# Optimization experiments

Hardware: AMD Instinct MI355X
Metric: run time of the kernel (lower is better)

Reference implementation:

```python
import jax, jax.numpy as jnp
import numpy as np

N = 500_000
EPS = 1e-5  # torch BatchNorm1d default eps

def _lin(x, w, b):
    # Conv1d(k=1) / Linear over per-point features: x [N,Cin], w [Cout,Cin]
    return x @ w.T + b

def _bn(x, g, b):
    # training-mode BatchNorm1d with batch=1: stats over the N points per channel
    m = jnp.mean(x, axis=0)
    v = jnp.mean((x - m) ** 2, axis=0)  # biased variance, as torch uses for normalization
    return g * (x - m) * jax.lax.rsqrt(v + EPS) + b

def _fuse(f3d, f2d, w2d, b2d, w3d, b3d, watt, batt):
    # AttentionalFuser: tanh/sigmoid gated fusion, output channels = 2*C
    d2d = _lin(f2d, w2d, b2d)                      # [N,C]
    mid = jnp.tanh(_lin(f3d, w3d, b3d) + d2d)      # [N,C]
    att = jax.nn.sigmoid(_lin(mid, watt, batt))    # [N,C]
    return jnp.concatenate([f3d, att * d2d], axis=1)  # [N,2C]

def setup_inputs() -> dict:
    key = jax.random.key(0)
    ks = iter(jax.random.split(key, 64))
    def rn(*shape):
        return jax.random.normal(next(ks), shape, dtype=jnp.float32) * 0.1
    inp = {"points": jax.random.normal(next(ks), (N, 10), dtype=jnp.float32)}
    for i, c in zip(range(1, 5), [8, 16, 32, 64]):
        inp[f"f2d_{i}"] = jax.random.normal(next(ks), (N, c), dtype=jnp.float32)
    for i, (o, ci) in enumerate([(8, 6), (16, 16), (32, 32), (64, 64), (256, 128)], 1):
        inp[f"w_c{i}"] = rn(o, ci); inp[f"b_c{i}"] = rn(o)
    for i, c in zip(range(1, 6), [16, 32, 64, 128, 256]):
        inp[f"g{i}"] = jnp.ones((c,), jnp.float32); inp[f"be{i}"] = jnp.zeros((c,), jnp.float32)
    for i, c in zip(range(1, 5), [8, 16, 32, 64]):
        inp[f"w2d_{i}"] = rn(c, c); inp[f"b2d_{i}"] = rn(c)
        inp[f"w3d_{i}"] = rn(c, c); inp[f"b3d_{i}"] = rn(c)
        inp[f"watt_{i}"] = rn(c, c); inp[f"batt_{i}"] = rn(c)
    return inp

def reference(points, f2d_1, f2d_2, f2d_3, f2d_4,
              w_c1, b_c1, w_c2, b_c2, w_c3, b_c3, w_c4, b_c4, w_c5, b_c5,
              g1, be1, g2, be2, g3, be3, g4, be4, g5, be5,
              w2d_1, b2d_1, w3d_1, b3d_1, watt_1, batt_1,
              w2d_2, b2d_2, w3d_2, b3d_2, watt_2, batt_2,
              w2d_3, b2d_3, w3d_3, b3d_3, watt_3, batt_3,
              w2d_4, b2d_4, w3d_4, b3d_4, watt_4, batt_4):
    x = jnp.concatenate([points[:, 0:3], points[:, 7:10]], axis=1)  # [N,6] pos+RGB
    x = jax.nn.relu(_lin(x, w_c1, b_c1))                            # [N,8]
    x = _bn(_fuse(x, f2d_1, w2d_1, b2d_1, w3d_1, b3d_1, watt_1, batt_1), g1, be1)  # [N,16]
    x = jax.nn.relu(_lin(x, w_c2, b_c2))                            # [N,16]
    x = _bn(_fuse(x, f2d_2, w2d_2, b2d_2, w3d_2, b3d_2, watt_2, batt_2), g2, be2)  # [N,32]
    x = jax.nn.relu(_lin(x, w_c3, b_c3))                            # [N,32]
    x = _bn(_fuse(x, f2d_3, w2d_3, b2d_3, w3d_3, b3d_3, watt_3, batt_3), g3, be3)  # [N,64]
    point_feature = x                                               # [N,64]
    x = jax.nn.relu(_lin(x, w_c4, b_c4))                            # [N,64]
    x = _bn(_fuse(x, f2d_4, w2d_4, b2d_4, w3d_4, b3d_4, watt_4, batt_4), g4, be4)  # [N,128]
    x = _bn(jax.nn.relu(_lin(x, w_c5, b_c5)), g5, be5)              # [N,256]
    glob = jnp.max(x, axis=0)                                       # [256] max-pool over points
    glob_rep = jnp.broadcast_to(glob[None, :], (points.shape[0], 256))
    out = jnp.concatenate([glob_rep, point_feature], axis=1)        # [N,320]
    return out.T[None]                                              # [1,320,N]
```

## Files before the change

### kernel.cpp

```cpp
#include <hip/hip_runtime.h>

#define EPSV 1e-5f
#define STS 1536

typedef short bf16x8 __attribute__((ext_vector_type(8)));
typedef _Float16 f16x8 __attribute__((ext_vector_type(8)));
typedef float f32x4  __attribute__((ext_vector_type(4)));
#define MFMA_B16(a,b,c) __builtin_amdgcn_mfma_f32_16x16x32_bf16(a,b,c,0,0,0)
#define MFMA_F16(a,b,c) __builtin_amdgcn_mfma_f32_16x16x32_f16(a,b,c,0,0,0)

__device__ __forceinline__ unsigned short f2bf(float x){
  unsigned u = __float_as_uint(x);
  return (unsigned short)((u + 0x7fffu + ((u >> 16) & 1u)) >> 16);
}
__device__ __forceinline__ float bf2f(unsigned short h){ return __uint_as_float((unsigned)h << 16); }
__device__ __forceinline__ unsigned short f2h(float x){
  union { _Float16 h; unsigned short u; } cv; cv.h = (_Float16)x; return cv.u;
}
__device__ __forceinline__ float h2f(unsigned short u){
  union { _Float16 h; unsigned short u; } cv; cv.u = u; return (float)cv.h;
}

__device__ __forceinline__ float wredsum(float v){
  #pragma unroll
  for (int o = 32; o > 0; o >>= 1) v += __shfl_xor(v, o, 64);
  return v;
}
__device__ __forceinline__ float fsig(float x){ return 1.0f / (1.0f + __expf(-x)); }
__device__ __forceinline__ float ftanh(float x){ return 1.0f - 2.0f / (__expf(2.0f * x) + 1.0f); }

__global__ __launch_bounds__(256) void k_wprep(
    const float* __restrict__ wc4, const float* __restrict__ w2d4,
    const float* __restrict__ w3d4, const float* __restrict__ wat4,
    const float* __restrict__ w5, unsigned short* __restrict__ wbf)
{
  int i = (blockIdx.x * 256 + threadIdx.x) * 4;
  const float* src; int base;
  if      (i < 4096){  src = wc4;  base = 0; }
  else if (i < 8192){  src = w2d4; base = 4096; }
  else if (i < 12288){ src = w3d4; base = 8192; }
  else if (i < 16384){ src = wat4; base = 12288; }
  else              {  src = w5;   base = 16384; }
  float4 v = *(const float4*)(src + (i - base));
  ushort4 o;
  o.x = f2bf(v.x); o.y = f2bf(v.y); o.z = f2bf(v.z); o.w = f2bf(v.w);
  *(ushort4*)(wbf + i) = o;
}

__global__ __launch_bounds__(256) void k_wprep2(
    const float* __restrict__ wc2, const float* __restrict__ w2d2,
    const float* __restrict__ w3d2, const float* __restrict__ wat2,
    const float* __restrict__ wc3, const float* __restrict__ w2d3,
    const float* __restrict__ w3d3, const float* __restrict__ wat3,
    unsigned short* __restrict__ wbf)
{
  const int t = threadIdx.x;
  for (int e = t; e < 2048; e += 256){
    int mat = e >> 9, idx = e & 511, m = idx >> 5, k = idx & 31;
    float v;
    if (mat == 1) v = (k >= 16) ? w2d2[m*16 + (k-16)] : 0.f;
    else {
      const float* w = (mat == 0) ? wc2 : (mat == 2) ? w3d2 : wat2;
      v = (k < 16) ? w[m*16 + k] : 0.f;
    }
    wbf[49152 + e] = f2h(v);
  }
  for (int e = t; e < 4096; e += 256){
    int mat = e >> 10, idx = e & 1023;
    const float* w = (mat == 0) ? wc3 : (mat == 1) ? w2d3 : (mat == 2) ? w3d3 : wat3;
    wbf[51200 + e] = f2h(w[idx]);
  }
}

__global__ __launch_bounds__(256) void k_stage1(
    const float* __restrict__ pts, const float* __restrict__ f2d,
    const float* __restrict__ Wc, const float* __restrict__ bc,
    const float* __restrict__ W2d, const float* __restrict__ b2d,
    const float* __restrict__ W3d, const float* __restrict__ b3d,
    const float* __restrict__ Watt, const float* __restrict__ batt,
    float* __restrict__ uout, float* __restrict__ gS, float* __restrict__ gQ,
    int ncopy, int N)
{
  const int tid = threadIdx.x;
  __shared__ float sW1[48], s2d[64], s3d[64], sat[64];
  __shared__ float sS[16], sQ[16];
  if (tid < 48)                 sW1[tid]       = Wc[tid];
  if (tid >= 64  && tid < 128)  s2d[tid - 64]  = W2d[tid - 64];
  if (tid >= 128 && tid < 192)  s3d[tid - 128] = W3d[tid - 128];
  if (tid >= 192)               sat[tid - 192] = Watt[tid - 192];
  if (tid < 16){ sS[tid] = 0.f; sQ[tid] = 0.f; }
  __syncthreads();

  float as[8], aq[8], as2[8], aq2[8];
  #pragma unroll
  for (int i = 0; i < 8; i++){ as[i]=0.f; aq[i]=0.f; as2[i]=0.f; aq2[i]=0.f; }

  for (int n0 = blockIdx.x * 256; n0 < N; n0 += gridDim.x * 256){
    const int n = n0 + tid;
    const bool act = n < N;
    const size_t nc = act ? (size_t)n : 0;

    const float* p = pts + nc * 10;
    float xin[6];
    xin[0]=p[0]; xin[1]=p[1]; xin[2]=p[2]; xin[3]=p[7]; xin[4]=p[8]; xin[5]=p[9];
    float x1[8];
    #pragma unroll
    for (int i = 0; i < 8; i++){
      float a = bc[i];
      #pragma unroll
      for (int j = 0; j < 6; j++) a = fmaf(sW1[i*6+j], xin[j], a);
      x1[i] = fmaxf(a, 0.f);
    }
    float f[8];
    { const float4* fp4 = (const float4*)(f2d + nc * 8);
      float4 t0 = fp4[0], t1 = fp4[1];
      f[0]=t0.x; f[1]=t0.y; f[2]=t0.z; f[3]=t0.w;
      f[4]=t1.x; f[5]=t1.y; f[6]=t1.z; f[7]=t1.w; }
    float d2d[8];
    #pragma unroll
    for (int i = 0; i < 8; i++){
      const float4* w = (const float4*)(s2d + i*8);
      float4 w0 = w[0], w1 = w[1];
      float a = b2d[i];
      a = fmaf(w0.x, f[0], a); a = fmaf(w0.y, f[1], a);
      a = fmaf(w0.z, f[2], a); a = fmaf(w0.w, f[3], a);
      a = fmaf(w1.x, f[4], a); a = fmaf(w1.y, f[5], a);
      a = fmaf(w1.z, f[6], a); a = fmaf(w1.w, f[7], a);
      d2d[i] = a;
    }
    float mid[8];
    #pragma unroll
    for (int i = 0; i < 8; i++){
      const float4* w = (const float4*)(s3d + i*8);
      float4 w0 = w[0], w1 = w[1];
      float a = b3d[i] + d2d[i];
      a = fmaf(w0.x, x1[0], a); a = fmaf(w0.y, x1[1], a);
      a = fmaf(w0.z, x1[2], a); a = fmaf(w0.w, x1[3], a);
      a = fmaf(w1.x, x1[4], a); a = fmaf(w1.y, x1[5], a);
      a = fmaf(w1.z, x1[6], a); a = fmaf(w1.w, x1[7], a);
      mid[i] = ftanh(a);
    }
    float r[8];
    #pragma unroll
    for (int i = 0; i < 8; i++){
      const float4* w = (const float4*)(sat + i*8);
      float4 w0 = w[0], w1 = w[1];
      float a = batt[i];
      a = fmaf(w0.x, mid[0], a); a = fmaf(w0.y, mid[1], a);
      a = fmaf(w0.z, mid[2], a); a = fmaf(w0.w, mid[3], a);
      a = fmaf(w1.x, mid[4], a); a = fmaf(w1.y, mid[5], a);
      a = fmaf(w1.z, mid[6], a); a = fmaf(w1.w, mid[7], a);
      r[i] = fsig(a) * d2d[i];
    }
    if (act){
      float* urow = uout + nc * 16;
      *(float4*)(urow + 0)  = make_float4(x1[0], x1[1], x1[2], x1[3]);
      *(float4*)(urow + 4)  = make_float4(x1[4], x1[5], x1[6], x1[7]);
      *(float4*)(urow + 8)  = make_float4(r[0], r[1], r[2], r[3]);
      *(float4*)(urow + 12) = make_float4(r[4], r[5], r[6], r[7]);
    }
    #pragma unroll
    for (int i = 0; i < 8; i++){
      float v = act ? x1[i] : 0.f;
      as[i] += v; aq[i] += v * v;
      float v2 = act ? r[i] : 0.f;
      as2[i] += v2; aq2[i] += v2 * v2;
    }
  }
  #pragma unroll
  for (int i = 0; i < 8; i++){
    float s = wredsum(as[i]), qv = wredsum(aq[i]);
    float s2 = wredsum(as2[i]), q2 = wredsum(aq2[i]);
    if ((tid & 63) == 0){
      atomicAdd(&sS[i], s);     atomicAdd(&sQ[i], qv);
      atomicAdd(&sS[8+i], s2);  atomicAdd(&sQ[8+i], q2);
    }
  }
  __syncthreads();
  if (tid < 16){
    const int co = (blockIdx.x & (ncopy - 1)) * STS;
    atomicAdd(&gS[co + tid], sS[tid]); atomicAdd(&gQ[co + tid], sQ[tid]);
  }
}

__global__ __launch_bounds__(256) void k_stage2_mfma(
    const float* __restrict__ u1, const float* __restrict__ pS, const float* __restrict__ pQ,
    const float* __restrict__ gam, const float* __restrict__ bet,
    const float* __restrict__ f2d,
    const unsigned short* __restrict__ wh,
    const float* __restrict__ bc, const float* __restrict__ b2d,
    const float* __restrict__ b3d, const float* __restrict__ batt,
    unsigned short* __restrict__ u2o, float* __restrict__ gS, float* __restrict__ gQ,
    int ncopy, float invN, int N)
{
  const int tid = threadIdx.x;
  __shared__ float sA[16], sB[16];
  __shared__ unsigned short yb[64*24], fb[64*24], xb[64*24], mb[64*24];
  __shared__ float sS[32], sQ[32];
  if (tid < 16){
    float s = 0.f, qv = 0.f;
    for (int c = 0; c < ncopy; c++){ s += pS[c*STS + tid]; qv += pQ[c*STS + tid]; }
    float m = s * invN;
    float v = qv * invN - m * m;
    float a = gam[tid] * rsqrtf(v + EPSV);
    sA[tid] = a; sB[tid] = fmaf(-a, m, bet[tid]);
  }
  if (tid < 32){ sS[tid] = 0.f; sQ[tid] = 0.f; }
  __syncthreads();

  const int w = tid >> 6;
  const int lane = tid & 63;
  const int cN = lane & 15;
  const int q = lane >> 4;
  const int brow = w*16 + cN;

  f16x8 aWc = *(const f16x8*)(wh + 0    + cN*32 + q*8);
  f16x8 aW2 = *(const f16x8*)(wh + 512  + cN*32 + q*8);
  f16x8 aW3 = *(const f16x8*)(wh + 1024 + cN*32 + q*8);
  f16x8 aWa = *(const f16x8*)(wh + 1536 + cN*32 + q*8);
  f32x4 bbc = *(const f32x4*)(bc   + q*4);
  f32x4 bb2 = *(const f32x4*)(b2d  + q*4);
  f32x4 bb3 = *(const f32x4*)(b3d  + q*4);
  f32x4 bba = *(const f32x4*)(batt + q*4);

  #define BF2(buf) (*(const f16x8*)(((q < 2) ? (buf) : fb) + brow*24 + (q & 1)*8))

  f32x4 ssx = {0,0,0,0}, qqx = {0,0,0,0};
  f32x4 ssr = {0,0,0,0}, qqr = {0,0,0,0};

  for (int pt0 = blockIdx.x * 64; pt0 < N; pt0 += gridDim.x * 64){
    {
      const int pt = tid >> 2, seg = tid & 3;
      const int gpt = pt0 + pt;
      const bool v = gpt < N;
      float4 t  = *(const float4*)(u1  + (size_t)(v ? gpt : 0) * 16 + seg*4);
      float4 ff = *(const float4*)(f2d + (size_t)(v ? gpt : 0) * 16 + seg*4);
      const float* a = sA + seg*4;
      const float* b = sB + seg*4;
      float y0 = v ? fmaf(a[0], t.x, b[0]) : 0.f;
      float y1 = v ? fmaf(a[1], t.y, b[1]) : 0.f;
      float y2 = v ? fmaf(a[2], t.z, b[2]) : 0.f;
      float y3 = v ? fmaf(a[3], t.w, b[3]) : 0.f;
      uint2 yw, fw;
      yw.x = (unsigned)f2h(y0) | ((unsigned)f2h(y1) << 16);
      yw.y = (unsigned)f2h(y2) | ((unsigned)f2h(y3) << 16);
      fw.x = (unsigned)f2h(v ? ff.x : 0.f) | ((unsigned)f2h(v ? ff.y : 0.f) << 16);
      fw.y = (unsigned)f2h(v ? ff.z : 0.f) | ((unsigned)f2h(v ? ff.w : 0.f) << 16);
      *(uint2*)(yb + pt*24 + seg*4) = yw;
      *(uint2*)(fb + pt*24 + seg*4) = fw;
    }
    __syncthreads();

    const bool vc = (pt0 + brow) < N;
    f16x8 Bv = BF2(yb);
    f32x4 accx = MFMA_F16(aWc, Bv, bbc);
    f32x4 accd = MFMA_F16(aW2, Bv, bb2);
    f32x4 xv;
    #pragma unroll
    for (int r = 0; r < 4; r++){
      float z = fmaxf(accx[r], 0.f);
      xv[r] = z;
      float zm = vc ? z : 0.f;
      ssx[r] += zm; qqx[r] += zm * zm;
    }
    uint2 pk;
    pk.x = (unsigned)f2h(xv[0]) | ((unsigned)f2h(xv[1]) << 16);
    pk.y = (unsigned)f2h(xv[2]) | ((unsigned)f2h(xv[3]) << 16);
    *(uint2*)(xb + brow*24 + q*4) = pk;
    if (vc) *(uint2*)(u2o + (size_t)(pt0 + brow) * 32 + q*4) = pk;
    __syncthreads();

    f32x4 accm = MFMA_F16(aW3, BF2(xb), bb3 + accd);
    #pragma unroll
    for (int r = 0; r < 4; r++) accm[r] = ftanh(accm[r]);
    pk.x = (unsigned)f2h(accm[0]) | ((unsigned)f2h(accm[1]) << 16);
    pk.y = (unsigned)f2h(accm[2]) | ((unsigned)f2h(accm[3]) << 16);
    *(uint2*)(mb + brow*24 + q*4) = pk;
    __syncthreads();

    f32x4 acca = MFMA_F16(aWa, BF2(mb), bba);
    f32x4 rv;
    #pragma unroll
    for (int r = 0; r < 4; r++){
      float rr = fsig(acca[r]) * accd[r];
      rv[r] = rr;
      float zm = vc ? rr : 0.f;
      ssr[r] += zm; qqr[r] += zm * zm;
    }
    if (vc){
      uint2 rk;
      rk.x = (unsigned)f2h(rv[0]) | ((unsigned)f2h(rv[1]) << 16);
      rk.y = (unsigned)f2h(rv[2]) | ((unsigned)f2h(rv[3]) << 16);
      *(uint2*)(u2o + (size_t)(pt0 + brow) * 32 + 16 + q*4) = rk;
    }
    __syncthreads();
  }
  #undef BF2

  #pragma unroll
  for (int r = 0; r < 4; r++){
    float s = ssx[r], qq = qqx[r], s2 = ssr[r], q2 = qqr[r];
    #pragma unroll
    for (int m = 1; m < 16; m <<= 1){
      s  += __shfl_xor(s,  m, 64); qq += __shfl_xor(qq, m, 64);
      s2 += __shfl_xor(s2, m, 64); q2 += __shfl_xor(q2, m, 64);
    }
    if (cN == 0){
      int ch = q*4 + r;
      atomicAdd(&sS[ch], s);       atomicAdd(&sQ[ch], qq);
      atomicAdd(&sS[16 + ch], s2); atomicAdd(&sQ[16 + ch], q2);
    }
  }
  __syncthreads();
  if (tid < 32){
    const int co = (blockIdx.x & (ncopy - 1)) * STS;
    atomicAdd(&gS[co + tid], sS[tid]); atomicAdd(&gQ[co + tid], sQ[tid]);
  }
}

__global__ __launch_bounds__(256) void k_stage3_mfma(
    const unsigned short* __restrict__ u2, const float* __restrict__ pS, const float* __restrict__ pQ,
    const float* __restrict__ gam, const float* __restrict__ bet,
    const float* __restrict__ f2d,
    const unsigned short* __restrict__ wh,
    const float* __restrict__ bc, const float* __restrict__ b2d,
    const float* __restrict__ b3d, const float* __restrict__ batt,
    unsigned short* __restrict__ u3o, float* __restrict__ gS, float* __restrict__ gQ,
    int ncopy, float invN, int N)
{
  const int tid = threadIdx.x;
  __shared__ float sA[32], sB[32];
  __shared__ unsigned short yb[64*40], fb[64*40], xb[64*40], mb[64*40];
  __shared__ float sS[64], sQ[64];
  if (tid < 32){
    float s = 0.f, qv = 0.f;
    for (int c = 0; c < ncopy; c++){ s += pS[c*STS + tid]; qv += pQ[c*STS + tid]; }
    float m = s * invN;
    float v = qv * invN - m * m;
    float a = gam[tid] * rsqrtf(v + EPSV);
    sA[tid] = a; sB[tid] = fmaf(-a, m, bet[tid]);
  }
  if (tid < 64){ sS[tid] = 0.f; sQ[tid] = 0.f; }
  __syncthreads();

  const int w = tid >> 6;
  const int lane = tid & 63;
  const int cN = lane & 15;
  const int q = lane >> 4;
  const int brow = w*16 + cN;

  f16x8 aWc[2], aW2[2], aW3[2], aWa[2];
  f32x4 bbc[2], bb2[2], bb3[2], bba[2];
  #pragma unroll
  for (int mg = 0; mg < 2; mg++){
    int off = (mg*16 + cN)*32 + q*8;
    aWc[mg] = *(const f16x8*)(wh + 0    + off);
    aW2[mg] = *(const f16x8*)(wh + 1024 + off);
    aW3[mg] = *(const f16x8*)(wh + 2048 + off);
    aWa[mg] = *(const f16x8*)(wh + 3072 + off);
    bbc[mg] = *(const f32x4*)(bc   + mg*16 + q*4);
    bb2[mg] = *(const f32x4*)(b2d  + mg*16 + q*4);
    bb3[mg] = *(const f32x4*)(b3d  + mg*16 + q*4);
    bba[mg] = *(const f32x4*)(batt + mg*16 + q*4);
  }

  #define BF3(buf) (*(const f16x8*)((buf) + brow*40 + q*8))

  f32x4 ssx[2], qqx[2], ssr[2], qqr[2];
  #pragma unroll
  for (int mg = 0; mg < 2; mg++){
    ssx[mg] = (f32x4){0,0,0,0}; qqx[mg] = (f32x4){0,0,0,0};
    ssr[mg] = (f32x4){0,0,0,0}; qqr[mg] = (f32x4){0,0,0,0};
  }

  for (int pt0 = blockIdx.x * 64; pt0 < N; pt0 += gridDim.x * 64){
    {
      const int pt = tid >> 2, seg = tid & 3;
      const int gpt = pt0 + pt;
      const bool v = gpt < N;
      uint4 t = *(const uint4*)(u2 + (size_t)(v ? gpt : 0) * 32 + seg*8);
      unsigned hw[4] = {t.x, t.y, t.z, t.w};
      unsigned ow[4];
      #pragma unroll
      for (int k = 0; k < 4; k++){
        int c0 = seg*8 + 2*k;
        float v0 = v ? fmaf(sA[c0],   h2f((unsigned short)(hw[k] & 0xffff)), sB[c0])   : 0.f;
        float v1 = v ? fmaf(sA[c0+1], h2f((unsigned short)(hw[k] >> 16)),    sB[c0+1]) : 0.f;
        ow[k] = (unsigned)f2h(v0) | ((unsigned)f2h(v1) << 16);
      }
      uint4 o; o.x = ow[0]; o.y = ow[1]; o.z = ow[2]; o.w = ow[3];
      *(uint4*)(yb + pt*40 + seg*8) = o;

      float4 f0 = *(const float4*)(f2d + (size_t)(v ? gpt : 0) * 32 + seg*8);
      float4 f1 = *(const float4*)(f2d + (size_t)(v ? gpt : 0) * 32 + seg*8 + 4);
      uint4 fo;
      fo.x = (unsigned)f2h(v ? f0.x : 0.f) | ((unsigned)f2h(v ? f0.y : 0.f) << 16);
      fo.y = (unsigned)f2h(v ? f0.z : 0.f) | ((unsigned)f2h(v ? f0.w : 0.f) << 16);
      fo.z = (unsigned)f2h(v ? f1.x : 0.f) | ((unsigned)f2h(v ? f1.y : 0.f) << 16);
      fo.w = (unsigned)f2h(v ? f1.z : 0.f) | ((unsigned)f2h(v ? f1.w : 0.f) << 16);
      *(uint4*)(fb + pt*40 + seg*8) = fo;
    }
    __syncthreads();

    const bool vc = (pt0 + brow) < N;
    f16x8 By = BF3(yb);
    f16x8 Bf = BF3(fb);
    f32x4 accd[2];
    #pragma unroll
    for (int mg = 0; mg < 2; mg++){
      f32x4 accx = MFMA_F16(aWc[mg], By, bbc[mg]);
      accd[mg]   = MFMA_F16(aW2[mg], Bf, bb2[mg]);
      f32x4 xv;
      #pragma unroll
      for (int r = 0; r < 4; r++){
        float z = fmaxf(accx[r], 0.f);
        xv[r] = z;
        float zm = vc ? z : 0.f;
        ssx[mg][r] += zm; qqx[mg][r] += zm * zm;
      }
      uint2 pk;
      pk.x = (unsigned)f2h(xv[0]) | ((unsigned)f2h(xv[1]) << 16);
      pk.y = (unsigned)f2h(xv[2]) | ((unsigned)f2h(xv[3]) << 16);
      *(uint2*)(xb + brow*40 + mg*16 + q*4) = pk;
      if (vc) *(uint2*)(u3o + (size_t)(pt0 + brow) * 64 + mg*16 + q*4) = pk;
    }
    __syncthreads();

    f16x8 Bx = BF3(xb);
    #pragma unroll
    for (int mg = 0; mg < 2; mg++){
      f32x4 accm = MFMA_F16(aW3[mg], Bx, bb3[mg] + accd[mg]);
      #pragma unroll
      for (int r = 0; r < 4; r++) accm[r] = ftanh(accm[r]);
      uint2 pk;
      pk.x = (unsigned)f2h(accm[0]) | ((unsigned)f2h(accm[1]) << 16);
      pk.y = (unsigned)f2h(accm[2]) | ((unsigned)f2h(accm[3]) << 16);
      *(uint2*)(mb + brow*40 + mg*16 + q*4) = pk;
    }
    __syncthreads();

    f16x8 Bm = BF3(mb);
    #pragma unroll
    for (int mg = 0; mg < 2; mg++){
      f32x4 acca = MFMA_F16(aWa[mg], Bm, bba[mg]);
      f32x4 rv;
      #pragma unroll
      for (int r = 0; r < 4; r++){
        float rr = fsig(acca[r]) * accd[mg][r];
        rv[r] = rr;
        float zm = vc ? rr : 0.f;
        ssr[mg][r] += zm; qqr[mg][r] += zm * zm;
      }
      if (vc){
        uint2 rk;
        rk.x = (unsigned)f2h(rv[0]) | ((unsigned)f2h(rv[1]) << 16);
        rk.y = (unsigned)f2h(rv[2]) | ((unsigned)f2h(rv[3]) << 16);
        *(uint2*)(u3o + (size_t)(pt0 + brow) * 64 + 32 + mg*16 + q*4) = rk;
      }
    }
  }
  #undef BF3

  #pragma unroll
  for (int mg = 0; mg < 2; mg++){
    #pragma unroll
    for (int r = 0; r < 4; r++){
      float s = ssx[mg][r], qq = qqx[mg][r], s2 = ssr[mg][r], q2 = qqr[mg][r];
      #pragma unroll
      for (int m = 1; m < 16; m <<= 1){
        s  += __shfl_xor(s,  m, 64); qq += __shfl_xor(qq, m, 64);
        s2 += __shfl_xor(s2, m, 64); q2 += __shfl_xor(q2, m, 64);
      }
      if (cN == 0){
        int ch = mg*16 + q*4 + r;
        atomicAdd(&sS[ch], s);       atomicAdd(&sQ[ch], qq);
        atomicAdd(&sS[32 + ch], s2); atomicAdd(&sQ[32 + ch], q2);
      }
    }
  }
  __syncthreads();
  if (tid < 64){
    const int co = (blockIdx.x & (ncopy - 1)) * STS;
    atomicAdd(&gS[co + tid], sS[tid]); atomicAdd(&gQ[co + tid], sQ[tid]);
  }
}

__global__ __launch_bounds__(256) void k_stage4_mfma(
    const unsigned short* __restrict__ u3, const float* __restrict__ pS, const float* __restrict__ pQ,
    const float* __restrict__ gam, const float* __restrict__ bet,
    const float* __restrict__ f2d,
    const unsigned short* __restrict__ wbf,
    const float* __restrict__ bc, const float* __restrict__ b2d,
    const float* __restrict__ b3d, const float* __restrict__ batt,
    unsigned short* __restrict__ u4o, float* __restrict__ gS, float* __restrict__ gQ,
    int ncopy, float invN, int N)
{
  const int tid = threadIdx.x;
  __shared__ float sA[64], sB[64];
  __shared__ unsigned short yb[64*72], fb[64*72], xb[64*72], mb[64*72], rb[64*72];

  if (tid < 64){
    float s = 0.f, qv = 0.f;
    for (int c = 0; c < ncopy; c++){ s += pS[c*STS + tid]; qv += pQ[c*STS + tid]; }
    float m = s * invN;
    float v = qv * invN - m * m;
    float a = gam[tid] * rsqrtf(v + EPSV);
    sA[tid] = a; sB[tid] = fmaf(-a, m, bet[tid]);
  }
  __syncthreads();

  const int w = tid >> 6;
  const int lane = tid & 63;
  const int cN = lane & 15;
  const int q = lane >> 4;

  bf16x8 aWc[2], aW2[2], aW3[2], aWa[2];
  #pragma unroll
  for (int kc = 0; kc < 2; kc++){
    size_t off = (size_t)(w*16 + cN) * 64 + kc*32 + q*8;
    aWc[kc] = *(const bf16x8*)(wbf + off);
    aW2[kc] = *(const bf16x8*)(wbf + 4096 + off);
    aW3[kc] = *(const bf16x8*)(wbf + 8192 + off);
    aWa[kc] = *(const bf16x8*)(wbf + 12288 + off);
  }
  f32x4 bbc = *(const f32x4*)(bc   + w*16 + q*4);
  f32x4 bb2 = *(const f32x4*)(b2d  + w*16 + q*4);
  f32x4 bb3 = *(const f32x4*)(b3d  + w*16 + q*4);
  f32x4 bba = *(const f32x4*)(batt + w*16 + q*4);

  #define BFRAG(buf, p, kc) (*(const bf16x8*)((buf) + ((p)*16 + cN)*72 + (kc)*32 + q*8))

  f32x4 ssx = {0,0,0,0}, qqx = {0,0,0,0};
  f32x4 ssr = {0,0,0,0}, qqr = {0,0,0,0};

  for (int pt0 = blockIdx.x * 64; pt0 < N; pt0 += gridDim.x * 64){
    {
      const int pt = tid >> 2;
      const int c16 = (tid & 3) << 4;
      const int gpt = pt0 + pt;
      const bool v = gpt < N;
      const unsigned short* ur = u3 + (size_t)(v ? gpt : 0) * 64 + c16;
      const float4* fr = (const float4*)(f2d + (size_t)(v ? gpt : 0) * 64 + c16);
      uint4 t0 = *(const uint4*)(ur);
      uint4 t1 = *(const uint4*)(ur + 8);
      unsigned hw[8] = {t0.x, t0.y, t0.z, t0.w, t1.x, t1.y, t1.z, t1.w};
      #pragma unroll
      for (int i = 0; i < 4; i++){
        float u0 = h2f((unsigned short)(hw[2*i] & 0xffff));
        float u1v = h2f((unsigned short)(hw[2*i] >> 16));
        float u2v = h2f((unsigned short)(hw[2*i+1] & 0xffff));
        float u3v = h2f((unsigned short)(hw[2*i+1] >> 16));
        float4 ff = fr[i];
        float4 a = *(const float4*)(sA + c16 + 4*i);
        float4 b = *(const float4*)(sB + c16 + 4*i);
        float y0 = v ? fmaf(a.x, u0, b.x) : 0.f;
        float y1 = v ? fmaf(a.y, u1v, b.y) : 0.f;
        float y2 = v ? fmaf(a.z, u2v, b.z) : 0.f;
        float y3 = v ? fmaf(a.w, u3v, b.w) : 0.f;
        uint2 yw, fw;
        yw.x = (unsigned)f2bf(y0) | ((unsigned)f2bf(y1) << 16);
        yw.y = (unsigned)f2bf(y2) | ((unsigned)f2bf(y3) << 16);
        fw.x = (unsigned)f2bf(v ? ff.x : 0.f) | ((unsigned)f2bf(v ? ff.y : 0.f) << 16);
        fw.y = (unsigned)f2bf(v ? ff.z : 0.f) | ((unsigned)f2bf(v ? ff.w : 0.f) << 16);
        *(uint2*)(yb + pt*72 + c16 + 4*i) = yw;
        *(uint2*)(fb + pt*72 + c16 + 4*i) = fw;
      }
    }
    __syncthreads();

    f32x4 d2d[4];
    #pragma unroll
    for (int p = 0; p < 4; p++){
      f32x4 acc = bb2;
      acc = MFMA_B16(aW2[0], BFRAG(fb, p, 0), acc);
      acc = MFMA_B16(aW2[1], BFRAG(fb, p, 1), acc);
      d2d[p] = acc;
    }
    #pragma unroll
    for (int p = 0; p < 4; p++){
      f32x4 acc = bbc;
      acc = MFMA_B16(aWc[0], BFRAG(yb, p, 0), acc);
      acc = MFMA_B16(aWc[1], BFRAG(yb, p, 1), acc);
      const bool vc = (pt0 + p*16 + cN) < N;
      #pragma unroll
      for (int r = 0; r < 4; r++){
        float z = fmaxf(acc[r], 0.f);
        acc[r] = z;
        float zm = vc ? z : 0.f;
        ssx[r] += zm; qqx[r] += zm * zm;
      }
      uint2 pk;
      pk.x = (unsigned)f2bf(acc[0]) | ((unsigned)f2bf(acc[1]) << 16);
      pk.y = (unsigned)f2bf(acc[2]) | ((unsigned)f2bf(acc[3]) << 16);
      *(uint2*)(xb + (p*16 + cN)*72 + w*16 + q*4) = pk;
    }
    __syncthreads();
    #pragma unroll
    for (int p = 0; p < 4; p++){
      f32x4 acc = bb3 + d2d[p];
      acc = MFMA_B16(aW3[0], BFRAG(xb, p, 0), acc);
      acc = MFMA_B16(aW3[1], BFRAG(xb, p, 1), acc);
      #pragma unroll
      for (int r = 0; r < 4; r++) acc[r] = ftanh(acc[r]);
      uint2 pk;
      pk.x = (unsigned)f2bf(acc[0]) | ((unsigned)f2bf(acc[1]) << 16);
      pk.y = (unsigned)f2bf(acc[2]) | ((unsigned)f2bf(acc[3]) << 16);
      *(uint2*)(mb + (p*16 + cN)*72 + w*16 + q*4) = pk;
    }
    __syncthreads();
    #pragma unroll
    for (int p = 0; p < 4; p++){
      f32x4 acc = bba;
      acc = MFMA_B16(aWa[0], BFRAG(mb, p, 0), acc);
      acc = MFMA_B16(aWa[1], BFRAG(mb, p, 1), acc);
// ... 136 lines not shown
        #pragma unroll
        for (int r = 0; r < 4; r++){
          float z = fmaxf(acc[r], 0.f);
          float zm = vc ? z : 0.f;
          s5[mg][r] += zm; q5[mg][r] += zm * zm;
          mx5[mg][r] = fmaxf(mx5[mg][r], zm);
          mn5[mg][r] = fminf(mn5[mg][r], vc ? z : FINF);
        }
      }
    }
    __syncthreads();
  }

  const int co = (blockIdx.x & (ncopy - 1)) * STS;
  #pragma unroll
  for (int mg = 0; mg < 4; mg++){
    #pragma unroll
    for (int r = 0; r < 4; r++){
      float s = s5[mg][r], qq = q5[mg][r], mx = mx5[mg][r], mn = mn5[mg][r];
      #pragma unroll
      for (int m = 1; m < 16; m <<= 1){
        s  += __shfl_xor(s,  m, 64); qq += __shfl_xor(qq, m, 64);
        mx = fmaxf(mx, __shfl_xor(mx, m, 64));
        mn = fminf(mn, __shfl_xor(mn, m, 64));
      }
      if (cN == 0){
        int ch = (w*4 + mg)*16 + q*4 + r;
        atomicAdd(&gS[co + ch], s); atomicAdd(&gQ[co + ch], qq);
        atomicMax(&gMx[co + ch], __float_as_int(mx));
        atomicMin(&gMn[co + ch], __float_as_int(mn));
      }
    }
  }
}

__global__ __launch_bounds__(256) void k_pf(
    const unsigned short* __restrict__ u3, const float* __restrict__ pS, const float* __restrict__ pQ,
    const float* __restrict__ gam, const float* __restrict__ bet,
    float* __restrict__ out, int ncopy, float invN, int N)
{
  const int tid = threadIdx.x;
  const int n0 = blockIdx.x * 64;
  __shared__ float sA[64], sB[64];
  __shared__ float T[64][68];
  if (tid < 64){
    float s = 0.f, qv = 0.f;
    for (int c = 0; c < ncopy; c++){ s += pS[c*STS + tid]; qv += pQ[c*STS + tid]; }
    float m = s * invN;
    float v = qv * invN - m * m;
    float a = gam[tid] * rsqrtf(v + EPSV);
    sA[tid] = a; sB[tid] = fmaf(-a, m, bet[tid]);
  }
  __syncthreads();
  {
    const int r = tid >> 2;
    const int c16 = (tid & 3) << 4;
    const int gn = n0 + r;
    const bool v = gn < N;
    const unsigned short* ur = u3 + (size_t)(v ? gn : 0) * 64 + c16;
    uint4 t0 = *(const uint4*)(ur);
    uint4 t1 = *(const uint4*)(ur + 8);
    unsigned hw[8] = {t0.x, t0.y, t0.z, t0.w, t1.x, t1.y, t1.z, t1.w};
    #pragma unroll
    for (int i = 0; i < 4; i++){
      float u0 = h2f((unsigned short)(hw[2*i] & 0xffff));
      float u1v = h2f((unsigned short)(hw[2*i] >> 16));
      float u2v = h2f((unsigned short)(hw[2*i+1] & 0xffff));
      float u3v = h2f((unsigned short)(hw[2*i+1] >> 16));
      float4 a = *(const float4*)(sA + c16 + 4*i);
      float4 b = *(const float4*)(sB + c16 + 4*i);
      T[c16 + 4*i + 0][r] = v ? fmaf(a.x, u0, b.x) : 0.f;
      T[c16 + 4*i + 1][r] = v ? fmaf(a.y, u1v, b.y) : 0.f;
      T[c16 + 4*i + 2][r] = v ? fmaf(a.z, u2v, b.z) : 0.f;
      T[c16 + 4*i + 3][r] = v ? fmaf(a.w, u3v, b.w) : 0.f;
    }
  }
  __syncthreads();
  {
    const int ch = tid >> 2;
    const int m16 = (tid & 3) << 4;
    #pragma unroll
    for (int i = 0; i < 4; i++){
      int nn = n0 + m16 + 4*i;
      if (nn < N)
        *(float4*)(out + (size_t)(256 + ch) * N + nn) = *(const float4*)(&T[ch][m16 + 4*i]);
    }
  }
}

__global__ __launch_bounds__(256) void k_fill(
    const float* __restrict__ gS, const float* __restrict__ gQ,
    const int* __restrict__ gMx, const int* __restrict__ gMn,
    const float* __restrict__ g5, const float* __restrict__ be5,
    float* __restrict__ out, int ncopy, float invN, int N)
{
  const int c = blockIdx.y;
  const float FINF = __int_as_float(0x7f800000);
  float s = 0.f, q = 0.f, zx = 0.f, zn = FINF;
  for (int cp = 0; cp < ncopy; cp++){
    s += gS[cp*STS + c]; q += gQ[cp*STS + c];
    zx = fmaxf(zx, __int_as_float(gMx[cp*STS + c]));
    zn = fminf(zn, __int_as_float(gMn[cp*STS + c]));
  }
  float m = s * invN;
  float v = q * invN - m * m;
  float a = g5[c] * rsqrtf(v + EPSV);
  float d = fmaf(-a, m, be5[c]);
  float glob = (a >= 0.f) ? fmaf(a, zx, d) : fmaf(a, zn, d);
  int n0 = (blockIdx.x * 256 + threadIdx.x) * 8;
  float4 gv = make_float4(glob, glob, glob, glob);
  if (n0 < N)     *(float4*)(out + (size_t)c * N + n0)     = gv;
  if (n0 + 4 < N) *(float4*)(out + (size_t)c * N + n0 + 4) = gv;
}

extern "C" void kernel_launch(void* const* d_in, const int* in_sizes, int n_in,
                              void* d_out, int out_size, void* d_ws, size_t ws_size,
                              hipStream_t stream) {
  const int N = in_sizes[0] / 10;
  auto F = [&](int i){ return (const float*)d_in[i]; };
  const float* P  = F(0);
  const float* F1 = F(1); const float* F2 = F(2); const float* F3 = F(3); const float* F4 = F(4);
  const float* Wc1 = F(5);  const float* Bc1 = F(6);
  const float* Wc2 = F(7);  const float* Bc2 = F(8);
  const float* Wc3 = F(9);  const float* Bc3 = F(10);
  const float* Wc4 = F(11); const float* Bc4 = F(12);
  const float* Wc5 = F(13); const float* Bc5 = F(14);
  const float* G1 = F(15); const float* BE1 = F(16);
  const float* G2 = F(17); const float* BE2 = F(18);
  const float* G3 = F(19); const float* BE3 = F(20);
  const float* G4 = F(21); const float* BE4 = F(22);
  const float* G5 = F(23); const float* BE5 = F(24);
  const float *W2d1=F(25), *B2d1=F(26), *W3d1=F(27), *B3d1=F(28), *Wat1=F(29), *Bat1=F(30);
  const float *W2d2=F(31), *B2d2=F(32), *W3d2=F(33), *B3d2=F(34), *Wat2=F(35), *Bat2=F(36);
  const float *W2d3=F(37), *B2d3=F(38), *W3d3=F(39), *B3d3=F(40), *Wat3=F(41), *Bat3=F(42);
  const float *W2d4=F(43), *B2d4=F(44), *W3d4=F(45), *B3d4=F(46), *Wat4=F(47), *Bat4=F(48);

  float* out = (float*)d_out;
  float* u1 = out;
  unsigned short* u2 = (unsigned short*)(out + (size_t)N * 16);
  unsigned short* u3 = (unsigned short*)(out + (size_t)N * 32);
  unsigned short* u4 = (unsigned short*)(out + (size_t)N * 64);

  unsigned short* wbf = (unsigned short*)d_ws;
  float* st = (float*)((char*)d_ws + 110592);
  const int ncopy = (ws_size >= (size_t)110592 + 8u * STS * sizeof(float)) ? 8 : 1;
  float* S1 = st;        float* Q1 = st + 16;
  float* S2 = st + 32;   float* Q2 = st + 64;
  float* S3 = st + 96;   float* Q3 = st + 160;
  float* S4 = st + 224;  float* Q4 = st + 352;
  float* S5 = st + 480;  float* Q5 = st + 736;
  int*   MX = (int*)(st + 992);
  int*   MN = (int*)(st + 1248);
  hipMemsetAsync(st, 0, (size_t)ncopy * STS * sizeof(float), stream);
  for (int c = 0; c < ncopy; c++)
    hipMemsetAsync(MN + c * STS, 0x7f, 256 * sizeof(float), stream);

  const int nb = (N + 255) / 256;
  const int nb64 = (N + 63) / 64;
  const float invN = 1.0f / (float)N;
  int NB1 = 1024; if (NB1 > nb) NB1 = nb;
  int NB2 = 1024; if (NB2 > nb64) NB2 = nb64;
  int NB3 = 768;  if (NB3 > nb64) NB3 = nb64;
  int NB4 = 768;  if (NB4 > nb64) NB4 = nb64;
  int NB5 = 1024; if (NB5 > nb64) NB5 = nb64;
  if (NB1 < 1) NB1 = 1; if (NB2 < 1) NB2 = 1; if (NB3 < 1) NB3 = 1;
  if (NB4 < 1) NB4 = 1; if (NB5 < 1) NB5 = 1;

  k_wprep<<<48, 256, 0, stream>>>(Wc4, W2d4, W3d4, Wat4, Wc5, wbf);
  k_wprep2<<<1, 256, 0, stream>>>(Wc2, W2d2, W3d2, Wat2, Wc3, W2d3, W3d3, Wat3, wbf);
  k_stage1<<<NB1, 256, 0, stream>>>(P, F1, Wc1, Bc1, W2d1, B2d1, W3d1, B3d1, Wat1, Bat1,
                                    u1, S1, Q1, ncopy, N);
  k_stage2_mfma<<<NB2, 256, 0, stream>>>(u1, S1, Q1, G1, BE1, F2, wbf + 49152,
                                         Bc2, B2d2, B3d2, Bat2,
                                         u2, S2, Q2, ncopy, invN, N);
  k_stage3_mfma<<<NB3, 256, 0, stream>>>(u2, S2, Q2, G2, BE2, F3, wbf + 51200,
                                         Bc3, B2d3, B3d3, Bat3,
                                         u3, S3, Q3, ncopy, invN, N);
  k_pf<<<nb64, 256, 0, stream>>>(u3, S3, Q3, G3, BE3, out, ncopy, invN, N);
  k_stage4_mfma<<<NB4, 256, 0, stream>>>(u3, S3, Q3, G3, BE3, F4, wbf,
                                         Bc4, B2d4, B3d4, Bat4,
                                         u4, S4, Q4, ncopy, invN, N);
  k_stage5_mfma<<<NB5, 256, 0, stream>>>(u4, S4, Q4, G4, BE4, wbf + 16384, Bc5,
                                         S5, Q5, MX, MN, ncopy, invN, N);
  dim3 gfill((N / 8 + 255) / 256, 256, 1);
  k_fill<<<gfill, 256, 0, stream>>>(S5, Q5, MX, MN, G5, BE5, out, ncopy, invN, N);
}
```

Measured before the change: 1.200 ms.

## Process more points per block in stages 2-3 and fold MN init into wprep

Stages 2 and 3 now handle 256 and 128 points per iteration, with each wave running several 16-point MFMA tiles between barriers. This cuts barrier and loop overhead per point and uses fuller per-thread row loads. Stage 2 changes its shared layout so the mid tensor shares a padded buffer with x, and the attention weight is zero-padded to match. The per-copy hipMemsetAsync calls for the min buffer are replaced by a loop inside k_wprep2, removing extra launches. Shared memory per block grows, which may reduce occupancy.

```diff
diff --git a/kernel.cpp b/kernel.cpp
--- a/kernel.cpp
+++ b/kernel.cpp
@@ -52,23 +52,25 @@
     const float* __restrict__ w3d2, const float* __restrict__ wat2,
     const float* __restrict__ wc3, const float* __restrict__ w2d3,
     const float* __restrict__ w3d3, const float* __restrict__ wat3,
-    unsigned short* __restrict__ wbf)
+    unsigned short* __restrict__ wbf, int* __restrict__ mn, int ncopy)
 {
   const int t = threadIdx.x;
   for (int e = t; e < 2048; e += 256){
     int mat = e >> 9, idx = e & 511, m = idx >> 5, k = idx & 31;
+    const float* w = (mat == 0) ? wc2 : (mat == 1) ? w2d2 : (mat == 2) ? w3d2 : wat2;
     float v;
-    if (mat == 1) v = (k >= 16) ? w2d2[m*16 + (k-16)] : 0.f;
-    else {
-      const float* w = (mat == 0) ? wc2 : (mat == 2) ? w3d2 : wat2;
-      v = (k < 16) ? w[m*16 + k] : 0.f;
-    }
+    if (mat == 1 || mat == 3) v = (k >= 16) ? w[m*16 + (k-16)] : 0.f;
+    else                      v = (k < 16)  ? w[m*16 + k]      : 0.f;
     wbf[49152 + e] = f2h(v);
   }
   for (int e = t; e < 4096; e += 256){
     int mat = e >> 10, idx = e & 1023;
     const float* w = (mat == 0) ? wc3 : (mat == 1) ? w2d3 : (mat == 2) ? w3d3 : wat3;
     wbf[51200 + e] = f2h(w[idx]);
+  }
+  for (int e = t; e < ncopy * 256; e += 256){
+    int c = e >> 8, i = e & 255;
+    mn[c*STS + i] = 0x7f7f7f7f;
   }
 }
 
@@ -195,7 +197,8 @@
 {
   const int tid = threadIdx.x;
   __shared__ float sA[16], sB[16];
-  __shared__ unsigned short yb[64*24], fb[64*24], xb[64*24], mb[64*24];
+  __shared__ unsigned short pb[256*40];
+  __shared__ unsigned short xm[256*40];
   __shared__ float sS[32], sQ[32];
   if (tid < 16){
     float s = 0.f, qv = 0.f;
@@ -206,13 +209,17 @@
     sA[tid] = a; sB[tid] = fmaf(-a, m, bet[tid]);
   }
   if (tid < 32){ sS[tid] = 0.f; sQ[tid] = 0.f; }
+  {
+    uint4 z = {0,0,0,0};
+    *(uint4*)(xm + tid*40 + 16) = z;
+    *(uint4*)(xm + tid*40 + 24) = z;
+  }
   __syncthreads();
 
   const int w = tid >> 6;
   const int lane = tid & 63;
   const int cN = lane & 15;
   const int q = lane >> 4;
-  const int brow = w*16 + cN;
 
   f16x8 aWc = *(const f16x8*)(wh + 0    + cN*32 + q*8);
   f16x8 aW2 = *(const f16x8*)(wh + 512  + cN*32 + q*8);
@@ -223,79 +230,103 @@
   f32x4 bb3 = *(const f32x4*)(b3d  + q*4);
   f32x4 bba = *(const f32x4*)(batt + q*4);
 
-  #define BF2(buf) (*(const f16x8*)(((q < 2) ? (buf) : fb) + brow*24 + (q & 1)*8))
-
   f32x4 ssx = {0,0,0,0}, qqx = {0,0,0,0};
   f32x4 ssr = {0,0,0,0}, qqr = {0,0,0,0};
 
-  for (int pt0 = blockIdx.x * 64; pt0 < N; pt0 += gridDim.x * 64){
+  for (int pt0 = blockIdx.x * 256; pt0 < N; pt0 += gridDim.x * 256){
     {
-      const int pt = tid >> 2, seg = tid & 3;
-      const int gpt = pt0 + pt;
+      const int gpt = pt0 + tid;
       const bool v = gpt < N;
-      float4 t  = *(const float4*)(u1  + (size_t)(v ? gpt : 0) * 16 + seg*4);
-      float4 ff = *(const float4*)(f2d + (size_t)(v ? gpt : 0) * 16 + seg*4);
-      const float* a = sA + seg*4;
-      const float* b = sB + seg*4;
-      float y0 = v ? fmaf(a[0], t.x, b[0]) : 0.f;
-      float y1 = v ? fmaf(a[1], t.y, b[1]) : 0.f;
-      float y2 = v ? fmaf(a[2], t.z, b[2]) : 0.f;
-      float y3 = v ? fmaf(a[3], t.w, b[3]) : 0.f;
-      uint2 yw, fw;
-      yw.x = (unsigned)f2h(y0) | ((unsigned)f2h(y1) << 16);
-      yw.y = (unsigned)f2h(y2) | ((unsigned)f2h(y3) << 16);
-      fw.x = (unsigned)f2h(v ? ff.x : 0.f) | ((unsigned)f2h(v ? ff.y : 0.f) << 16);
-      fw.y = (unsigned)f2h(v ? ff.z : 0.f) | ((unsigned)f2h(v ? ff.w : 0.f) << 16);
-      *(uint2*)(yb + pt*24 + seg*4) = yw;
-      *(uint2*)(fb + pt*24 + seg*4) = fw;
-    }
-    __syncthreads();
-
-    const bool vc = (pt0 + brow) < N;
-    f16x8 Bv = BF2(yb);
-    f32x4 accx = MFMA_F16(aWc, Bv, bbc);
-    f32x4 accd = MFMA_F16(aW2, Bv, bb2);
-    f32x4 xv;
-    #pragma unroll
-    for (int r = 0; r < 4; r++){
-      float z = fmaxf(accx[r], 0.f);
-      xv[r] = z;
-      float zm = vc ? z : 0.f;
-      ssx[r] += zm; qqx[r] += zm * zm;
-    }
-    uint2 pk;
-    pk.x = (unsigned)f2h(xv[0]) | ((unsigned)f2h(xv[1]) << 16);
-    pk.y = (unsigned)f2h(xv[2]) | ((unsigned)f2h(xv[3]) << 16);
-    *(uint2*)(xb + brow*24 + q*4) = pk;
-    if (vc) *(uint2*)(u2o + (size_t)(pt0 + brow) * 32 + q*4) = pk;
-    __syncthreads();
-
-    f32x4 accm = MFMA_F16(aW3, BF2(xb), bb3 + accd);
-    #pragma unroll
-    for (int r = 0; r < 4; r++) accm[r] = ftanh(accm[r]);
-    pk.x = (unsigned)f2h(accm[0]) | ((unsigned)f2h(accm[1]) << 16);
-    pk.y = (unsigned)f2h(accm[2]) | ((unsigned)f2h(accm[3]) << 16);
-    *(uint2*)(mb + brow*24 + q*4) = pk;
-    __syncthreads();
-
-    f32x4 acca = MFMA_F16(aWa, BF2(mb), bba);
-    f32x4 rv;
-    #pragma unroll
-    for (int r = 0; r < 4; r++){
-      float rr = fsig(acca[r]) * accd[r];
-      rv[r] = rr;
-      float zm = vc ? rr : 0.f;
-      ssr[r] += zm; qqr[r] += zm * zm;
-    }
-    if (vc){
-      uint2 rk;
-      rk.x = (unsigned)f2h(rv[0]) | ((unsigned)f2h(rv[1]) << 16);
-      rk.y = (unsigned)f2h(rv[2]) | ((unsigned)f2h(rv[3]) << 16);
-      *(uint2*)(u2o + (size_t)(pt0 + brow) * 32 + 16 + q*4) = rk;
-    }
-    __syncthreads();
-  }
-  #undef BF2
+      const float* ur = u1  + (size_t)(v ? gpt : 0) * 16;
+      const float* fr = f2d + (size_t)(v ? gpt : 0) * 16;
+      unsigned yw[8], fw[8];
+      #pragma unroll
+      for (int i = 0; i < 4; i++){
+        float4 t  = *(const float4*)(ur + 4*i);
+        float4 ff = *(const float4*)(fr + 4*i);
+        const float* a = sA + 4*i;
+        const float* b = sB + 4*i;
+        float y0 = v ? fmaf(a[0], t.x, b[0]) : 0.f;
+        float y1 = v ? fmaf(a[1], t.y, b[1]) : 0.f;
+        float y2 = v ? fmaf(a[2], t.z, b[2]) : 0.f;
+        float y3 = v ? fmaf(a[3], t.w, b[3]) : 0.f;
+        yw[2*i]   = (unsigned)f2h(y0) | ((unsigned)f2h(y1) << 16);
+        yw[2*i+1] = (unsigned)f2h(y2) | ((unsigned)f2h(y3) << 16);
+        fw[2*i]   = (unsigned)f2h(v ? ff.x : 0.f) | ((unsigned)f2h(v ? ff.y : 0.f) << 16);
+        fw[2*i+1] = (unsigned)f2h(v ? ff.z : 0.f) | ((unsigned)f2h(v ? ff.w : 0.f) << 16);
+      }
+      uint4 o;
+      o.x = yw[0]; o.y = yw[1]; o.z = yw[2]; o.w = yw[3];
+      *(uint4*)(pb + tid*40 + 0) = o;
+      o.x = yw[4]; o.y = yw[5]; o.z = yw[6]; o.w = yw[7];
+      *(uint4*)(pb + tid*40 + 8) = o;
+      o.x = fw[0]; o.y = fw[1]; o.z = fw[2]; o.w = fw[3];
+      *(uint4*)(pb + tid*40 + 16) = o;
+      o.x = fw[4]; o.y = fw[5]; o.z = fw[6]; o.w = fw[7];
+      *(uint4*)(pb + tid*40 + 24) = o;
+    }
+    __syncthreads();
+
+    f32x4 d2d[4];
+    #pragma unroll
+    for (int j = 0; j < 4; j++){
+      const int prow = (w*4 + j)*16 + cN;
+      f16x8 Bv = *(const f16x8*)(pb + prow*40 + q*8);
+      f32x4 accx = MFMA_F16(aWc, Bv, bbc);
+      d2d[j] = MFMA_F16(aW2, Bv, bb2);
+      const bool vc = (pt0 + prow) < N;
+      f32x4 xv;
+      #pragma unroll
+      for (int r = 0; r < 4; r++){
+        float z = fmaxf(accx[r], 0.f);
+        xv[r] = z;
+        float zm = vc ? z : 0.f;
+        ssx[r] += zm; qqx[r] += zm * zm;
+      }
+      uint2 pk;
+      pk.x = (unsigned)f2h(xv[0]) | ((unsigned)f2h(xv[1]) << 16);
+      pk.y = (unsigned)f2h(xv[2]) | ((unsigned)f2h(xv[3]) << 16);
+      *(uint2*)(xm + prow*40 + q*4) = pk;
+      if (vc) *(uint2*)(u2o + (size_t)(pt0 + prow) * 32 + q*4) = pk;
+    }
+    __syncthreads();
+
+    #pragma unroll
+    for (int j = 0; j < 4; j++){
+      const int prow = (w*4 + j)*16 + cN;
+      f16x8 Bx = *(const f16x8*)(xm + prow*40 + q*8);
+      f32x4 accm = MFMA_F16(aW3, Bx, bb3 + d2d[j]);
+      #pragma unroll
+      for (int r = 0; r < 4; r++) accm[r] = ftanh(accm[r]);
+      uint2 pk;
+      pk.x = (unsigned)f2h(accm[0]) | ((unsigned)f2h(accm[1]) << 16);
+      pk.y = (unsigned)f2h(accm[2]) | ((unsigned)f2h(accm[3]) << 16);
+      *(uint2*)(xm + prow*40 + 16 + q*4) = pk;
+    }
+    __syncthreads();
+
+    #pragma unroll
+    for (int j = 0; j < 4; j++){
+      const int prow = (w*4 + j)*16 + cN;
+      f16x8 Bm = *(const f16x8*)(xm + prow*40 + q*8);
+      f32x4 acca = MFMA_F16(aWa, Bm, bba);
+      const bool vc = (pt0 + prow) < N;
+      f32x4 rv;
+      #pragma unroll
+      for (int r = 0; r < 4; r++){
+        float rr = fsig(acca[r]) * d2d[j][r];
+        rv[r] = rr;
+        float zm = vc ? rr : 0.f;
+        ssr[r] += zm; qqr[r] += zm * zm;
+      }
+      if (vc){
+        uint2 rk;
+        rk.x = (unsigned)f2h(rv[0]) | ((unsigned)f2h(rv[1]) << 16);
+        rk.y = (unsigned)f2h(rv[2]) | ((unsigned)f2h(rv[3]) << 16);
+        *(uint2*)(u2o + (size_t)(pt0 + prow) * 32 + 16 + q*4) = rk;
+      }
+    }
+  }
 
   #pragma unroll
   for (int r = 0; r < 4; r++){
@@ -330,7 +361,7 @@
 {
   const int tid = threadIdx.x;
   __shared__ float sA[32], sB[32];
-  __shared__ unsigned short yb[64*40], fb[64*40], xb[64*40], mb[64*40];
+  __shared__ unsigned short yb[128*40], fb[128*40], xb[128*40], mb[128*40];
   __shared__ float sS[64], sQ[64];
   if (tid < 32){
     float s = 0.f, qv = 0.f;
@@ -347,7 +378,6 @@
   const int lane = tid & 63;
   const int cN = lane & 15;
   const int q = lane >> 4;
-  const int brow = w*16 + cN;
 
   f16x8 aWc[2], aW2[2], aW3[2], aWa[2];
   f32x4 bbc[2], bb2[2], bb3[2], bba[2];
@@ -364,8 +394,6 @@
     bba[mg] = *(const f32x4*)(batt + mg*16 + q*4);
   }
 
-  #define BF3(buf) (*(const f16x8*)((buf) + brow*40 + q*8))
-
   f32x4 ssx[2], qqx[2], ssr[2], qqr[2];
   #pragma unroll
   for (int mg = 0; mg < 2; mg++){
@@ -373,93 +401,119 @@
     ssr[mg] = (f32x4){0,0,0,0}; qqr[mg] = (f32x4){0,0,0,0};
   }
 
-  for (int pt0 = blockIdx.x * 64; pt0 < N; pt0 += gridDim.x * 64){
+  for (int pt0 = blockIdx.x * 128; pt0 < N; pt0 += gridDim.x * 128){
     {
-      const int pt = tid >> 2, seg = tid & 3;
+      const int pt = tid >> 1, h = tid & 1;
       const int gpt = pt0 + pt;
       const bool v = gpt < N;
-      uint4 t = *(const uint4*)(u2 + (size_t)(v ? gpt : 0) * 32 + seg*8);
-      unsigned hw[4] = {t.x, t.y, t.z, t.w};
-      unsigned ow[4];
+      const unsigned short* ur = u2 + (size_t)(v ? gpt : 0) * 32 + h*16;
+      uint4 t0 = *(const uint4*)(ur);
+      uint4 t1 = *(const uint4*)(ur + 8);
+      unsigned hw[4] = {t0.x, t0.y, t0.z, t0.w};
+      unsigned hw2[4] = {t1.x, t1.y, t1.z, t1.w};
+      unsigned ow[8];
       #pragma unroll
       for (int k = 0; k < 4; k++){
-        int c0 = seg*8 + 2*k;
+        int c0 = h*16 + 2*k;
         float v0 = v ? fmaf(sA[c0],   h2f((unsigned short)(hw[k] & 0xffff)), sB[c0])   : 0.f;
         float v1 = v ? fmaf(sA[c0+1], h2f((unsigned short)(hw[k] >> 16)),    sB[c0+1]) : 0.f;
         ow[k] = (unsigned)f2h(v0) | ((unsigned)f2h(v1) << 16);
-      }
-      uint4 o; o.x = ow[0]; o.y = ow[1]; o.z = ow[2]; o.w = ow[3];
-      *(uint4*)(yb + pt*40 + seg*8) = o;
-
-      float4 f0 = *(const float4*)(f2d + (size_t)(v ? gpt : 0) * 32 + seg*8);
-      float4 f1 = *(const float4*)(f2d + (size_t)(v ? gpt : 0) * 32 + seg*8 + 4);
-      uint4 fo;
-      fo.x = (unsigned)f2h(v ? f0.x : 0.f) | ((unsigned)f2h(v ? f0.y : 0.f) << 16);
-      fo.y = (unsigned)f2h(v ? f0.z : 0.f) | ((unsigned)f2h(v ? f0.w : 0.f) << 16);
-      fo.z = (unsigned)f2h(v ? f1.x : 0.f) | ((unsigned)f2h(v ? f1.y : 0.f) << 16);
-      fo.w = (unsigned)f2h(v ? f1.z : 0.f) | ((unsigned)f2h(v ? f1.w : 0.f) << 16);
-      *(uint4*)(fb + pt*40 + seg*8) = fo;
-    }
-    __syncthreads();
-
-    const bool vc = (pt0 + brow) < N;
-    f16x8 By = BF3(yb);
-    f16x8 Bf = BF3(fb);
-    f32x4 accd[2];
-    #pragma unroll
-    for (int mg = 0; mg < 2; mg++){
-      f32x4 accx = MFMA_F16(aWc[mg], By, bbc[mg]);
-      accd[mg]   = MFMA_F16(aW2[mg], Bf, bb2[mg]);
-      f32x4 xv;
-      #pragma unroll
-      for (int r = 0; r < 4; r++){
-        float z = fmaxf(accx[r], 0.f);
-        xv[r] = z;
-        float zm = vc ? z : 0.f;
-        ssx[mg][r] += zm; qqx[mg][r] += zm * zm;
-      }
-      uint2 pk;
-      pk.x = (unsigned)f2h(xv[0]) | ((unsigned)f2h(xv[1]) << 16);
-      pk.y = (unsigned)f2h(xv[2]) | ((unsigned)f2h(xv[3]) << 16);
-      *(uint2*)(xb + brow*40 + mg*16 + q*4) = pk;
-      if (vc) *(uint2*)(u3o + (size_t)(pt0 + brow) * 64 + mg*16 + q*4) = pk;
-    }
-    __syncthreads();
-
-    f16x8 Bx = BF3(xb);
-    #pragma unroll
-    for (int mg = 0; mg < 2; mg++){
-      f32x4 accm = MFMA_F16(aW3[mg], Bx, bb3[mg] + accd[mg]);
-      #pragma unroll
-      for (int r = 0; r < 4; r++) accm[r] = ftanh(accm[r]);
-      uint2 pk;
-      pk.x = (unsigned)f2h(accm[0]) | ((unsigned)f2h(accm[1]) << 16);
-      pk.y = (unsigned)f2h(accm[2]) | ((unsigned)f2h(accm[3]) << 16);
-      *(uint2*)(mb + brow*40 + mg*16 + q*4) = pk;
-    }
-    __syncthreads();
-
-    f16x8 Bm = BF3(mb);
-    #pragma unroll
-    for (int mg = 0; mg < 2; mg++){
-      f32x4 acca = MFMA_F16(aWa[mg], Bm, bba[mg]);
-      f32x4 rv;
-      #pragma unroll
-      for (int r = 0; r < 4; r++){
-        float rr = fsig(acca[r]) * accd[mg][r];
-        rv[r] = rr;
-        float zm = vc ? rr : 0.f;
-        ssr[mg][r] += zm; qqr[mg][r] += zm * zm;
-      }
-      if (vc){
-        uint2 rk;
-        rk.x = (unsigned)f2h(rv[0]) | ((unsigned)f2h(rv[1]) << 16);
-        rk.y = (unsigned)f2h(rv[2]) | ((unsigned)f2h(rv[3]) << 16);
-        *(uint2*)(u3o + (size_t)(pt0 + brow) * 64 + 32 + mg*16 + q*4) = rk;
-      }
-    }
-  }
-  #undef BF3
+        int c1 = h*16 + 8 + 2*k;
+        float v2 = v ? fmaf(sA[c1],   h2f((unsigned short)(hw2[k] & 0xffff)), sB[c1])   : 0.f;
+        float v3 = v ? fmaf(sA[c1+1], h2f((unsigned short)(hw2[k] >> 16)),    sB[c1+1]) : 0.f;
+        ow[4+k] = (unsigned)f2h(v2) | ((unsigned)f2h(v3) << 16);
+      }
+      uint4 o;
+      o.x = ow[0]; o.y = ow[1]; o.z = ow[2]; o.w = ow[3];
+      *(uint4*)(yb + pt*40 + h*16) = o;
+      o.x = ow[4]; o.y = ow[5]; o.z = ow[6]; o.w = ow[7];
+      *(uint4*)(yb + pt*40 + h*16 + 8) = o;
+
+      const float* fr = f2d + (size_t)(v ? gpt : 0) * 32 + h*16;
+      unsigned fo[8];
+      #pragma unroll
+      for (int i = 0; i < 4; i++){
+        float4 ff = *(const float4*)(fr + 4*i);
+        fo[2*i]   = (unsigned)f2h(v ? ff.x : 0.f) | ((unsigned)f2h(v ? ff.y : 0.f) << 16);
+        fo[2*i+1] = (unsigned)f2h(v ? ff.z : 0.f) | ((unsigned)f2h(v ? ff.w : 0.f) << 16);
+      }
+      o.x = fo[0]; o.y = fo[1]; o.z = fo[2]; o.w = fo[3];
+      *(uint4*)(fb + pt*40 + h*16) = o;
+      o.x = fo[4]; o.y = fo[5]; o.z = fo[6]; o.w = fo[7];
+      *(uint4*)(fb + pt*40 + h*16 + 8) = o;
+    }
+    __syncthreads();
+
+    f32x4 accd[2][2];
+    #pragma unroll
+    for (int j = 0; j < 2; j++){
+      const int prow = (w*2 + j)*16 + cN;
+      f16x8 By = *(const f16x8*)(yb + prow*40 + q*8);
+      f16x8 Bf = *(const f16x8*)(fb + prow*40 + q*8);
+      const bool vc = (pt0 + prow) < N;
+      #pragma unroll
+      for (int mg = 0; mg < 2; mg++){
+        f32x4 accx = MFMA_F16(aWc[mg], By, bbc[mg]);
+        accd[j][mg] = MFMA_F16(aW2[mg], Bf, bb2[mg]);
+        f32x4 xv;
+        #pragma unroll
+        for (int r = 0; r < 4; r++){
+          float z = fmaxf(accx[r], 0.f);
+          xv[r] = z;
+          float zm = vc ? z : 0.f;
+          ssx[mg][r] += zm; qqx[mg][r] += zm * zm;
+        }
+        uint2 pk;
+        pk.x = (unsigned)f2h(xv[0]) | ((unsigned)f2h(xv[1]) << 16);
+        pk.y = (unsigned)f2h(xv[2]) | ((unsigned)f2h(xv[3]) << 16);
+        *(uint2*)(xb + prow*40 + mg*16 + q*4) = pk;
+        if (vc) *(uint2*)(u3o + (size_t)(pt0 + prow) * 64 + mg*16 + q*4) = pk;
+      }
+    }
+    __syncthreads();
+
+    #pragma unroll
+    for (int j = 0; j < 2; j++){
+      const int prow = (w*2 + j)*16 + cN;
+      f16x8 Bx = *(const f16x8*)(xb + prow*40 + q*8);
+      #pragma unroll
+      for (int mg = 0; mg < 2; mg++){
+        f32x4 accm = MFMA_F16(aW3[mg], Bx, bb3[mg] + accd[j][mg]);
+        #pragma unroll
+        for (int r = 0; r < 4; r++) accm[r] = ftanh(accm[r]);
+        uint2 pk;
+        pk.x = (unsigned)f2h(accm[0]) | ((unsigned)f2h(accm[1]) << 16);
+        pk.y = (unsigned)f2h(accm[2]) | ((unsigned)f2h(accm[3]) << 16);
+        *(uint2*)(mb + prow*40 + mg*16 + q*4) = pk;
+      }
+    }
+    __syncthreads();
+
+    #pragma unroll
+    for (int j = 0; j < 2; j++){
+      const int prow = (w*2 + j)*16 + cN;
+      f16x8 Bm = *(const f16x8*)(mb + prow*40 + q*8);
+      const bool vc = (pt0 + prow) < N;
+      #pragma unroll
+      for (int mg = 0; mg < 2; mg++){
+        f32x4 acca = MFMA_F16(aWa[mg], Bm, bba[mg]);
+        f32x4 rv;
+        #pragma unroll
+        for (int r = 0; r < 4; r++){
+          float rr = fsig(acca[r]) * accd[j][mg][r];
+          rv[r] = rr;
+          float zm = vc ? rr : 0.f;
+          ssr[mg][r] += zm; qqr[mg][r] += zm * zm;
+        }
+        if (vc){
+          uint2 rk;
+          rk.x = (unsigned)f2h(rv[0]) | ((unsigned)f2h(rv[1]) << 16);
+          rk.y = (unsigned)f2h(rv[2]) | ((unsigned)f2h(rv[3]) << 16);
+          *(uint2*)(u3o + (size_t)(pt0 + prow) * 64 + 32 + mg*16 + q*4) = rk;
+        }
+      }
+    }
+  }
 
   #pragma unroll
   for (int mg = 0; mg < 2; mg++){
@@ -902,22 +956,22 @@
   int*   MX = (int*)(st + 992);
   int*   MN = (int*)(st + 1248);
   hipMemsetAsync(st, 0, (size_t)ncopy * STS * sizeof(float), stream);
-  for (int c = 0; c < ncopy; c++)
-    hipMemsetAsync(MN + c * STS, 0x7f, 256 * sizeof(float), stream);
 
   const int nb = (N + 255) / 256;
   const int nb64 = (N + 63) / 64;
+  const int nb128 = (N + 127) / 128;
   const float invN = 1.0f / (float)N;
   int NB1 = 1024; if (NB1 > nb) NB1 = nb;
-  int NB2 = 1024; if (NB2 > nb64) NB2 = nb64;
-  int NB3 = 768;  if (NB3 > nb64) NB3 = nb64;
+  int NB2 = 1024; if (NB2 > nb) NB2 = nb;
+  int NB3 = 1024; if (NB3 > nb128) NB3 = nb128;
   int NB4 = 768;  if (NB4 > nb64) NB4 = nb64;
   int NB5 = 1024; if (NB5 > nb64) NB5 = nb64;
   if (NB1 < 1) NB1 = 1; if (NB2 < 1) NB2 = 1; if (NB3 < 1) NB3 = 1;
   if (NB4 < 1) NB4 = 1; if (NB5 < 1) NB5 = 1;
 
   k_wprep<<<48, 256, 0, stream>>>(Wc4, W2d4, W3d4, Wat4, Wc5, wbf);
-  k_wprep2<<<1, 256, 0, stream>>>(Wc2, W2d2, W3d2, Wat2, Wc3, W2d3, W3d3, Wat3, wbf);
+  k_wprep2<<<1, 256, 0, stream>>>(Wc2, W2d2, W3d2, Wat2, Wc3, W2d3, W3d3, Wat3,
+                                  wbf, MN, ncopy);
   k_stage1<<<NB1, 256, 0, stream>>>(P, F1, Wc1, Bc1, W2d1, B2d1, W3d1, B3d1, Wat1, Bat1,
                                     u1, S1, Q1, ncopy, N);
   k_stage2_mfma<<<NB2, 256, 0, stream>>>(u1, S1, Q1, G1, BE1, F2, wbf + 49152,
```

New measurement: 1.212 ms. About the same (+1.0%).
